# Performance work log

Measured on AMD Instinct MI355X. Metric: run time of the kernel, lower is better.

The kernel has to match this reference:

```python
import jax, jax.numpy as jnp
import numpy as np
from jax import lax

DN = ('NCHW', 'OIHW', 'NCHW')

def conv(x, w, b, stride=1, pad=0):
    y = lax.conv_general_dilated(x, w, (stride, stride), ((pad, pad), (pad, pad)), dimension_numbers=DN)
    return y + b[None, :, None, None]

def conv_transpose(x, w, b):
    # torch ConvTranspose2d(k=4, s=2, p=1): w is (in_ch, out_ch, 4, 4)
    wf = jnp.flip(w, (2, 3)).transpose(1, 0, 2, 3)  # -> (out_ch, in_ch, 4, 4)
    pad = 4 - 1 - 1  # k - 1 - p = 2
    y = lax.conv_general_dilated(x, wf, (1, 1), ((pad, pad), (pad, pad)), lhs_dilation=(2, 2), dimension_numbers=DN)
    return y + b[None, :, None, None]

def setup_inputs() -> dict:
    key = jax.random.key(0)
    ks = jax.random.split(key, 16)
    HID, ZC, K = 256, 64, 512
    def w(k, shape):
        return (jax.random.normal(k, shape, jnp.float32) * 0.02)
    z = lambda n: jnp.zeros((n,), jnp.float32)
    return {
        'x': jax.random.uniform(ks[0], (8, 3, 128, 128), jnp.float32),
        'c1_w': w(ks[1], (HID, 3, 4, 4)), 'c1_b': z(HID),
        'c2_w': w(ks[2], (HID, HID, 4, 4)), 'c2_b': z(HID),
        'r0_w3': w(ks[3], (HID, HID, 3, 3)), 'r0_b3': z(HID),
        'r0_w1': w(ks[4], (HID, HID, 1, 1)), 'r0_b1': z(HID),
        'r1_w3': w(ks[5], (HID, HID, 3, 3)), 'r1_b3': z(HID),
        'r1_w1': w(ks[6], (HID, HID, 1, 1)), 'r1_b1': z(HID),
        'to_z_w': w(ks[7], (ZC, HID, 1, 1)), 'to_z_b': z(ZC),
        'codebook': jax.random.uniform(ks[8], (K, ZC), jnp.float32, -1.0 / K, 1.0 / K),
        'from_z_w': w(ks[9], (HID, ZC, 1, 1)), 'from_z_b': z(HID),
        't1_w': w(ks[10], (HID, HID, 4, 4)), 't1_b': z(HID),
        't2_w': w(ks[11], (HID, 3, 4, 4)), 't2_b': z(3),
    }

def _vqvae(x, c1_w, c1_b, c2_w, c2_b, r0_w3, r0_b3, r0_w1, r0_b1,
           r1_w3, r1_b3, r1_w1, r1_b1, to_z_w, to_z_b, codebook,
           from_z_w, from_z_b, t1_w, t1_b, t2_w, t2_b):
    # ---- Encoder ----
    h = jax.nn.relu(conv(x, c1_w, c1_b, stride=2, pad=1))
    h = jax.nn.relu(conv(h, c2_w, c2_b, stride=2, pad=1))
    for (w3, b3, w1, b1) in ((r0_w3, r0_b3, r0_w1, r0_b1), (r1_w3, r1_b3, r1_w1, r1_b1)):
        r = conv(jax.nn.relu(h), w3, b3, pad=1)
        r = conv(jax.nn.relu(r), w1, b1)
        h = h + r
    z_e = conv(h, to_z_w, to_z_b)  # [B, ZC, H/4, W/4]
    # ---- Vector quantization ----
    B, C, H, W = z_e.shape
    z_flat = z_e.transpose(0, 2, 3, 1).reshape(-1, C)  # [N, C]
    dist = (jnp.sum(z_flat * z_flat, axis=1, keepdims=True)
            - 2.0 * z_flat @ codebook.T
            + jnp.sum(codebook * codebook, axis=1)[None, :])  # [N, K]
    ids = jnp.argmin(dist, axis=1)  # [N]
    e_k_flat = codebook[ids]  # [N, C]
    e_k_st_flat = z_flat + lax.stop_gradient(e_k_flat - z_flat)
    e_k = e_k_flat.reshape(B, H, W, C).transpose(0, 3, 1, 2)
    e_k_st = e_k_st_flat.reshape(B, H, W, C).transpose(0, 3, 1, 2)
    ids = ids.reshape(B, H, W)
    # ---- Decoder ----
    d = jax.nn.relu(conv(e_k_st, from_z_w, from_z_b))
    d = jax.nn.relu(conv_transpose(d, t1_w, t1_b))
    out = jax.nn.sigmoid(conv_transpose(d, t2_w, t2_b))
    return out, z_e, e_k, ids

def reference(x, c1_w, c1_b, c2_w, c2_b, r0_w3, r0_b3, r0_w1, r0_b1,
              r1_w3, r1_b3, r1_w1, r1_b1, to_z_w, to_z_b, codebook,
              from_z_w, from_z_b, t1_w, t1_b, t2_w, t2_b):
    return _vqvae(x, c1_w, c1_b, c2_w, c2_b, r0_w3, r0_b3, r0_w1, r0_b1,
                  r1_w3, r1_b3, r1_w1, r1_b1, to_z_w, to_z_b, codebook,
                  from_z_w, from_z_b, t1_w, t1_b, t2_w, t2_b)
```

## Files before the change

kernel.cpp:

```cpp
#include <hip/hip_runtime.h>
#include <math.h>


typedef unsigned int uint;
typedef unsigned short ushort_t;
using short8 = __attribute__((ext_vector_type(8))) short;
using f32x4  = __attribute__((ext_vector_type(4))) float;

__device__ __attribute__((aligned(16))) ushort_t g_zpad[512];

static __device__ __forceinline__ int rfl(int x) { return __builtin_amdgcn_readfirstlane(x); }
static __device__ __forceinline__ ushort_t f2bf(float f) {
  uint u = __float_as_uint(f);
  return (ushort_t)((u + 0x7fffu + ((u >> 16) & 1u)) >> 16);
}
static __device__ __forceinline__ float bf2f(ushort_t b) {
  return __uint_as_float(((uint)b) << 16);
}
static __device__ __forceinline__ void gload16(const ushort_t* g, void* l) {
  __builtin_amdgcn_global_load_lds(
      (const __attribute__((address_space(1))) void*)g,
      (__attribute__((address_space(3))) void*)l, 16, 0, 0);
}

__global__ void k_transpose_w(const float* __restrict__ w, float* __restrict__ wT, int CO, int CIKK) {
  int idx = blockIdx.x * 256 + threadIdx.x;
  if (idx >= CO * CIKK) return;
  int co = idx % CO, i = idx / CO;
  wT[idx] = w[co * CIKK + i];
}

template<int KIND>
__global__ __launch_bounds__(256) void k_prep_enc(
    const float* __restrict__ w, ushort_t* __restrict__ wp)
{
  constexpr int KK = (KIND == 0) ? 16 : (KIND == 1 ? 9 : 1);
  constexpr int KW = (KIND == 0) ? 4  : (KIND == 1 ? 3 : 1);
  constexpr int NT = KK;
  const int tid = threadIdx.x;
  const int wvg = blockIdx.x * 4 + (tid >> 6);
  const int lane = tid & 63;
  const int co = wvg >> 2;
  const int ci = (wvg & 3) * 64 + lane;
  const float* src = w + (size_t)(co * 256 + ci) * KK;
  const int coT = co >> 6, row = co & 63, cg = ci >> 5, k = ci & 31;
  float v[KK];
#pragma unroll
  for (int j = 0; j < KK; ++j) v[j] = src[j];
#pragma unroll
  for (int tap = 0; tap < NT; ++tap) {
    int ky, kx;
    if (KIND == 0)      { ky = tap >> 2; kx = tap & 3; }
    else if (KIND == 1) { ky = tap / 3;  kx = tap - ky * 3; }
    else                { ky = 0; kx = 0; }
    float val = v[ky * KW + kx];
    ushort_t b0 = f2bf(val);
    ushort_t b1 = f2bf(val - bf2f(b0));
    const int chunk = tap * 8 + cg;
    size_t base = ((size_t)(chunk * 4 + coT) << 12) + row * 32 + k;
    wp[base] = b0;
    wp[base + 2048] = b1;
  }
}

__global__ void k_prep_t1w(const float* __restrict__ w, ushort_t* __restrict__ wb) {
  int idx = blockIdx.x * 256 + threadIdx.x;
  int kk  = idx & 31;
  int co  = (idx >> 5) & 255;
  int c8  = (idx >> 13) & 7;
  int tap = (idx >> 16) & 3;
  int par = idx >> 18;
  int ry = par & 1, rx = (par >> 1) & 1;
  int a = tap >> 1, b = tap & 1;
  int ky = ((ry + 1) & 1) + 2 * a;
  int kx = ((rx + 1) & 1) + 2 * b;
  int ci = c8 * 32 + kk;
  wb[idx] = f2bf(w[((ci * 256 + co) << 4) + ky * 4 + kx]);
}

__global__ void k_prep_t2w(const float* __restrict__ w, ushort_t* __restrict__ wb) {
  int idx = blockIdx.x * 256 + threadIdx.x;
  int k = idx & 31, co = (idx >> 5) & 15, chunk = (idx >> 9) & 31, par = idx >> 14;
  int tap = chunk >> 3, cg = chunk & 7;
  int a = tap >> 1, b = tap & 1;
  int ry = par & 1, rx = (par >> 1) & 1;
  int ky = ((ry + 1) & 1) + 2 * a;
  int kx = ((rx + 1) & 1) + 2 * b;
  int ci = cg * 32 + k;
  float v = (co < 3) ? w[((ci * 3 + co) << 4) + ky * 4 + kx] : 0.f;
  wb[idx] = f2bf(v);
}

__global__ void k_prep_cb(const float* __restrict__ cb, float* __restrict__ cnorm) {
  int idx = blockIdx.x * 256 + threadIdx.x;
  if (idx < 512) {
    float s = 0.f;
    for (int c = 0; c < 64; ++c) { float v = cb[idx * 64 + c]; s = fmaf(v, v, s); }
    cnorm[idx] = s;
  }
}

__global__ __launch_bounds__(256) void k_conv1_split(
    const float* __restrict__ in, ushort_t* __restrict__ o0, ushort_t* __restrict__ o1,
    const float* __restrict__ wT, const float* __restrict__ bias)
{
  __shared__ float s_in[3 * 360];
  const int tid = threadIdx.x;
  const int lane = tid & 63;
  const int wv = rfl(tid >> 6);
  const int px = lane & 7, py = lane >> 3;
  const int tx = blockIdx.x & 7, ty = blockIdx.x >> 3;
  const int X = tx * 8, Y = ty * 8;
  const int cob = blockIdx.y * 64 + wv * 16;
  const int n = blockIdx.z;
  float acc[16];
#pragma unroll
  for (int i = 0; i < 16; ++i) acc[i] = bias[cob + i];
  const float* inN = in + (size_t)n * 3 * 16384;
  for (int e = tid; e < 3 * 360; e += 256) {
    int col2 = e % 20; int t = e / 20; int row = t % 18; int ci = t / 18;
    int pr = col2 / 10, hc = col2 % 10, ixl = 2 * hc + pr;
    int iy = 2 * Y - 1 + row, ix = 2 * X - 1 + ixl;
    float v = 0.f;
    if (ixl < 18 && (unsigned)iy < 128u && (unsigned)ix < 128u)
      v = inN[ci * 16384 + iy * 128 + ix];
    s_in[e] = v;
  }
  __syncthreads();
  const float* wc = wT + cob;
#pragma unroll
  for (int c = 0; c < 3; ++c) {
    const float* base = s_in + c * 360 + py * 40 + px;
#pragma unroll
    for (int ky = 0; ky < 4; ++ky) {
#pragma unroll
      for (int kx = 0; kx < 4; ++kx) {
        float iv = base[ky * 20 + (kx & 1) * 10 + (kx >> 1)];
        const float* w = wc + (size_t)(c * 16 + ky * 4 + kx) * 256;
#pragma unroll
        for (int i = 0; i < 16; ++i) acc[i] = fmaf(iv, w[i], acc[i]);
      }
    }
  }
  const int pxg = n * 4096 + (Y + py) * 64 + (X + px);
  uint p0[8], p1[8];
#pragma unroll
  for (int i = 0; i < 8; ++i) {
    float va = fmaxf(acc[2 * i], 0.f), vb = fmaxf(acc[2 * i + 1], 0.f);
    ushort_t a0 = f2bf(va), b0 = f2bf(vb);
    ushort_t a1 = f2bf(va - bf2f(a0)), b1 = f2bf(vb - bf2f(b0));
    p0[i] = (uint)a0 | ((uint)b0 << 16);
    p1[i] = (uint)a1 | ((uint)b1 << 16);
  }
  ushort_t* d0 = o0 + (size_t)pxg * 256 + cob;
  ushort_t* d1 = o1 + (size_t)pxg * 256 + cob;
  uint4 v0a; v0a.x = p0[0]; v0a.y = p0[1]; v0a.z = p0[2]; v0a.w = p0[3];
  uint4 v0b; v0b.x = p0[4]; v0b.y = p0[5]; v0b.z = p0[6]; v0b.w = p0[7];
  uint4 v1a; v1a.x = p1[0]; v1a.y = p1[1]; v1a.z = p1[2]; v1a.w = p1[3];
  uint4 v1b; v1b.x = p1[4]; v1b.y = p1[5]; v1b.z = p1[6]; v1b.w = p1[7];
  *(uint4*)d0 = v0a; *(uint4*)(d0 + 8) = v0b;
  *(uint4*)d1 = v1a; *(uint4*)(d1 + 8) = v1b;
}

template<int KIND>
__global__ __launch_bounds__(256) void k_enc_mfma_split(
    const ushort_t* __restrict__ x0, const ushort_t* __restrict__ x1,
    const ushort_t* __restrict__ wp, float* __restrict__ part)
{
  __shared__ ushort_t smem[2][12288];
  const int tid = threadIdx.x, lane = tid & 63, wv = tid >> 6;
  const int l15 = lane & 15, q = lane >> 4;
  const int pxT = blockIdx.x, coT = blockIdx.y;
  constexpr int NCH = (KIND == 0) ? 128 : 72;
  const int CH0 = blockIdx.z * (NCH / 2), CH1 = CH0 + NCH / 2;
  f32x4 acc[4][2];
#pragma unroll
  for (int m = 0; m < 4; ++m)
#pragma unroll
    for (int n = 0; n < 2; ++n) acc[m][n] = (f32x4){0.f, 0.f, 0.f, 0.f};

  const int r0 = tid >> 2, kq = tid & 3;
  int bimg[2], bu[2], bvc[2];
#pragma unroll
  for (int r = 0; r < 2; ++r) {
    int bpx = pxT * 128 + r0 + r * 64;
    bimg[r] = bpx >> 10; int bp = bpx & 1023; bu[r] = bp >> 5; bvc[r] = bp & 31;
  }
  const ushort_t* srcB[2][2];
  int ptap = -1;
  auto retap = [&](int tap) {
    ptap = tap;
    int ky, kx;
    if (KIND == 0) { ky = tap >> 2; kx = tap & 3; }
    else           { ky = tap / 3;  kx = tap - ky * 3; }
#pragma unroll
    for (int r = 0; r < 2; ++r) {
      bool v; size_t rowb;
      if (KIND == 0) {
        int iy = 2 * bu[r] - 1 + ky, ix = 2 * bvc[r] - 1 + kx;
        v = ((unsigned)iy < 64u) && ((unsigned)ix < 64u);
        rowb = ((size_t)(bimg[r] * 4096 + iy * 64 + ix)) << 8;
      } else {
        int iy = bu[r] - 1 + ky, ix = bvc[r] - 1 + kx;
        v = ((unsigned)iy < 32u) && ((unsigned)ix < 32u);
        rowb = ((size_t)(bimg[r] * 1024 + iy * 32 + ix)) << 8;
      }
      srcB[r][0] = (v ? (x0 + rowb) : g_zpad) + kq * 8;
      srcB[r][1] = (v ? (x1 + rowb) : g_zpad) + kq * 8;
    }
  };

  const int wvb = wv * 1024;
  auto stage = [&](int chunk, int bi) {
    const int tap = chunk >> 3, cg = chunk & 7;
    if (tap != ptap) retap(tap);
    char* bufb = (char*)smem[bi];
    const ushort_t* ap = wp + ((size_t)(chunk * 4 + coT) << 12) + tid * 8;
    gload16(ap,        bufb + wvb);
    gload16(ap + 2048, bufb + 4096 + wvb);
    const int ko = cg * 32;
    gload16(srcB[0][0] + ko, bufb + 8192 + wvb);
    gload16(srcB[1][0] + ko, bufb + 8192 + 4096 + wvb);
    gload16(srcB[0][1] + ko, bufb + 16384 + wvb);
    gload16(srcB[1][1] + ko, bufb + 16384 + 4096 + wvb);
  };
  auto compute = [&](const ushort_t* buf) {
    const ushort_t* sA = buf;
    const ushort_t* sB = buf + 4096;
    short8 af[4][2], bf[2][2];
#pragma unroll
    for (int m = 0; m < 4; ++m)
#pragma unroll
      for (int pl = 0; pl < 2; ++pl)
        af[m][pl] = *(const short8*)(sA + pl * 2048 + (m * 16 + l15) * 32 + q * 8);
#pragma unroll
    for (int n = 0; n < 2; ++n)
#pragma unroll
      for (int pl = 0; pl < 2; ++pl)
        bf[n][pl] = *(const short8*)(sB + pl * 4096 + (wv * 32 + n * 16 + l15) * 32 + q * 8);
#pragma unroll
    for (int m = 0; m < 4; ++m)
#pragma unroll
      for (int n = 0; n < 2; ++n) {
        acc[m][n] = __builtin_amdgcn_mfma_f32_16x16x32_bf16(af[m][0], bf[n][0], acc[m][n], 0, 0, 0);
        acc[m][n] = __builtin_amdgcn_mfma_f32_16x16x32_bf16(af[m][0], bf[n][1], acc[m][n], 0, 0, 0);
        acc[m][n] = __builtin_amdgcn_mfma_f32_16x16x32_bf16(af[m][1], bf[n][0], acc[m][n], 0, 0, 0);
      }
  };

  stage(CH0, 0);
  __syncthreads();
  int cur = 0;
  for (int c = CH0; c < CH1; ++c) {
    if (c + 1 < CH1) stage(c + 1, cur ^ 1);
    compute(smem[cur]);
    __syncthreads();
    cur ^= 1;
  }

  float* pz = part + ((size_t)blockIdx.z << 21);
#pragma unroll
  for (int m = 0; m < 4; ++m) {
#pragma unroll
    for (int n = 0; n < 2; ++n) {
#pragma unroll
      for (int r = 0; r < 4; ++r) {
        const int co_l = m * 16 + q * 4 + r;
        const int px_l = wv * 32 + n * 16 + l15;
        const int px = pxT * 128 + px_l;
        const int img = px >> 10, pp = px & 1023;
        const size_t ha = ((size_t)(img * 256 + coT * 64 + co_l)) * 1024 + pp;
        pz[ha] = acc[m][n][r];
      }
    }
  }
}

template<bool WH>
__global__ __launch_bounds__(256) void k_enc_epi(
    const float* __restrict__ part, float* __restrict__ h32,
    ushort_t* __restrict__ s0, ushort_t* __restrict__ s1,
    const float* __restrict__ bias)
{
  const int px = blockIdx.x * 256 + threadIdx.x;
  const int co0 = blockIdx.y * 16;
  const int img = px >> 10, pp = px & 1023;
  const float* part1 = part + (1u << 21);
  uint p0[8], p1[8];
#pragma unroll
  for (int i = 0; i < 8; ++i) {
    size_t ha = ((size_t)(img * 256 + co0 + 2 * i)) * 1024 + pp;
    size_t hb = ha + 1024;
    float va = part[ha] + part1[ha] + bias[co0 + 2 * i];
    float vb = part[hb] + part1[hb] + bias[co0 + 2 * i + 1];
    float sa, sb;
    if (WH) {
      va = fmaxf(va, 0.f); vb = fmaxf(vb, 0.f);
      h32[ha] = va; h32[hb] = vb; sa = va; sb = vb;
    } else { sa = fmaxf(va, 0.f); sb = fmaxf(vb, 0.f); }
    ushort_t a0 = f2bf(sa), b0 = f2bf(sb);
    p0[i] = (uint)a0 | ((uint)b0 << 16);
    p1[i] = (uint)f2bf(sa - bf2f(a0)) | ((uint)f2bf(sb - bf2f(b0)) << 16);
  }
  ushort_t* d0 = s0 + (size_t)px * 256 + co0;
  ushort_t* d1 = s1 + (size_t)px * 256 + co0;
  uint4 v0a; v0a.x = p0[0]; v0a.y = p0[1]; v0a.z = p0[2]; v0a.w = p0[3];
  uint4 v0b; v0b.x = p0[4]; v0b.y = p0[5]; v0b.z = p0[6]; v0b.w = p0[7];
  uint4 v1a; v1a.x = p1[0]; v1a.y = p1[1]; v1a.z = p1[2]; v1a.w = p1[3];
  uint4 v1b; v1b.x = p1[4]; v1b.y = p1[5]; v1b.z = p1[6]; v1b.w = p1[7];
  *(uint4*)d0 = v0a; *(uint4*)(d0 + 8) = v0b;
  *(uint4*)d1 = v1a; *(uint4*)(d1 + 8) = v1b;
}

template<bool WS>
__global__ __launch_bounds__(256) void k_enc_mfma(
    const ushort_t* __restrict__ x0, const ushort_t* __restrict__ x1,
    const ushort_t* __restrict__ wp, const float* __restrict__ bias,
    float* __restrict__ h32, ushort_t* __restrict__ sp0, ushort_t* __restrict__ sp1)
{
  __shared__ ushort_t smem[24576];
  const int tid = threadIdx.x, lane = tid & 63, wv = tid >> 6;
  const int l15 = lane & 15, q = lane >> 4;
  const int pxT = blockIdx.x, coT = blockIdx.y;
  f32x4 acc[4][2];
#pragma unroll
  for (int m = 0; m < 4; ++m)
#pragma unroll
    for (int n = 0; n < 2; ++n) acc[m][n] = (f32x4){0.f, 0.f, 0.f, 0.f};

  const int r0 = tid >> 2, kq = tid & 3;
  const ushort_t* srcB[2][2];
#pragma unroll
  for (int r = 0; r < 2; ++r) {
    size_t rowb = ((size_t)(pxT * 128 + r0 + r * 64)) << 8;
    srcB[r][0] = x0 + rowb + kq * 8;
    srcB[r][1] = x1 + rowb + kq * 8;
  }
  const int wvb = wv * 1024;
  auto stage = [&](int c, int bi) {
    char* bufb = (char*)(smem + bi * 12288);
    const ushort_t* ap = wp + ((size_t)(c * 4 + coT) << 12) + tid * 8;
    gload16(ap,        bufb + wvb);
    gload16(ap + 2048, bufb + 4096 + wvb);
    const int ko = c * 32;
    gload16(srcB[0][0] + ko, bufb + 8192 + wvb);
    gload16(srcB[1][0] + ko, bufb + 8192 + 4096 + wvb);
    gload16(srcB[0][1] + ko, bufb + 16384 + wvb);
    gload16(srcB[1][1] + ko, bufb + 16384 + 4096 + wvb);
  };
  auto compute = [&](const ushort_t* buf) {
    const ushort_t* sA = buf;
    const ushort_t* sB = buf + 4096;
    short8 af[4][2], bf[2][2];
#pragma unroll
    for (int m = 0; m < 4; ++m)
#pragma unroll
      for (int pl = 0; pl < 2; ++pl)
        af[m][pl] = *(const short8*)(sA + pl * 2048 + (m * 16 + l15) * 32 + q * 8);
#pragma unroll
    for (int n = 0; n < 2; ++n)
#pragma unroll
      for (int pl = 0; pl < 2; ++pl)
        bf[n][pl] = *(const short8*)(sB + pl * 4096 + (wv * 32 + n * 16 + l15) * 32 + q * 8);
#pragma unroll
    for (int m = 0; m < 4; ++m)
#pragma unroll
      for (int n = 0; n < 2; ++n) {
        acc[m][n] = __builtin_amdgcn_mfma_f32_16x16x32_bf16(af[m][0], bf[n][0], acc[m][n], 0, 0, 0);
        acc[m][n] = __builtin_amdgcn_mfma_f32_16x16x32_bf16(af[m][0], bf[n][1], acc[m][n], 0, 0, 0);
        acc[m][n] = __builtin_amdgcn_mfma_f32_16x16x32_bf16(af[m][1], bf[n][0], acc[m][n], 0, 0, 0);
      }
  };

  stage(0, 0);
  __syncthreads();
  int cur = 0;
  for (int c = 0; c < 8; ++c) {
    if (c + 1 < 8) stage(c + 1, cur ^ 1);
    compute(smem + cur * 12288);
    __syncthreads();
    cur ^= 1;
  }

#pragma unroll
  for (int m = 0; m < 4; ++m) {
#pragma unroll
    for (int n = 0; n < 2; ++n) {
#pragma unroll
      for (int r = 0; r < 4; ++r) {
        const int co_l = m * 16 + q * 4 + r;
        const int px_l = wv * 32 + n * 16 + l15;
        float v = acc[m][n][r] + bias[coT * 64 + co_l];
        const int px = pxT * 128 + px_l;
        const int img = px >> 10, pp = px & 1023;
        const size_t ha = ((size_t)(img * 256 + coT * 64 + co_l)) * 1024 + pp;
        v += h32[ha];
        h32[ha] = v;
        if (WS) {
          float sv = fmaxf(v, 0.f);
          ushort_t b0 = f2bf(sv);
          smem[px_l * 72 + co_l] = b0;
          smem[9216 + px_l * 72 + co_l] = f2bf(sv - bf2f(b0));
        }
      }
    }
  }
  if (WS) {
    __syncthreads();
#pragma unroll
    for (int i = 0; i < 8; ++i) {
      int idx = tid + 256 * i;
      int pl = idx >> 10, w2 = idx & 1023, pxl = w2 >> 3, g = w2 & 7;
      uint4 vv = *(const uint4*)(smem + pl * 9216 + pxl * 72 + g * 8);
      ushort_t* dst = (pl ? sp1 : sp0) + ((size_t)(pxT * 128 + pxl)) * 256 + coT * 64 + g * 8;
      *(uint4*)dst = vv;
    }
  }
}

__global__ __launch_bounds__(256) void k_conv1x1(
    const float* __restrict__ in, float* __restrict__ out,
    const float* __restrict__ wT, const float* __restrict__ bias,
    int CI, int CO, int P)
{
  const int p = blockIdx.x * 256 + threadIdx.x;
  const int cob = blockIdx.y * 16;
  const int n = blockIdx.z;
  const float* inN = in + (size_t)n * CI * P + p;
  float acc[16];
#pragma unroll
  for (int i = 0; i < 16; ++i) acc[i] = bias[cob + i];
  const float* wr = wT + cob;
#pragma unroll 4
  for (int ci = 0; ci < CI; ++ci) {
    float iv = inN[(size_t)ci * P];
    const float* w = wr + (size_t)ci * CO;
#pragma unroll
    for (int i = 0; i < 16; ++i) acc[i] = fmaf(iv, w[i], acc[i]);
  }
  float* outN = out + (size_t)n * CO * P + p;
#pragma unroll
  for (int i = 0; i < 16; ++i) outN[(size_t)(cob + i) * P] = acc[i];
}

__global__ __launch_bounds__(256) void k_vq_part(
    const float* __restrict__ z_e, const float* __restrict__ cb,
    const float* __restrict__ cnorm, float* __restrict__ pbest, int* __restrict__ pbid)
{
  int g = blockIdx.x * 256 + threadIdx.x;
  int chunk = blockIdx.y;
  int img = g >> 10, p = g & 1023;
  const float* zp = z_e + (size_t)img * 64 * 1024 + p;
  float z[64];
#pragma unroll
  for (int c = 0; c < 64; ++c) z[c] = zp[(size_t)c * 1024];
  float best = 3.4e38f; int bid = chunk << 5;
  const int j0 = chunk << 5;
  for (int j = j0; j < j0 + 32; ++j) {
    const float* cj = cb + j * 64;
    float m = 0.f;
#pragma unroll
    for (int c = 0; c < 64; ++c) m = fmaf(z[c], cj[c], m);
    float d = fmaf(-2.f, m, cnorm[j]);
    if (d < best) { best = d; bid = j; }
  }
  pbest[chunk * 8192 + g] = best;
  pbid[chunk * 8192 + g] = bid;
}

__global__ __launch_bounds__(256) void k_vq_reduce(
    const float* __restrict__ pbest, const int* __restrict__ pbid,
    const float* __restrict__ cb, float* __restrict__ ids_f, float* __restrict__ ek)
{
  int g = blockIdx.x * 256 + threadIdx.x;
  float best = 3.4e38f; int bid = 0;
#pragma unroll
  for (int ch = 0; ch < 16; ++ch) {
    float d = pbest[ch * 8192 + g];
    int b = pbid[ch * 8192 + g];
    if (d < best) { best = d; bid = b; }
  }
  ids_f[g] = (float)bid;
  int img = g >> 10, p = g & 1023;
  const float* cbid = cb + bid * 64;
  float* ekp = ek + (size_t)img * 64 * 1024 + p;
#pragma unroll
  for (int c = 0; c < 64; ++c) ekp[(size_t)c * 1024] = cbid[c];
}

__global__ __launch_bounds__(256) void k_from_z(
    const float* __restrict__ ek, ushort_t* __restrict__ nhwc,
    const float* __restrict__ wT, const float* __restrict__ bias)
{
  const int p = blockIdx.x * 256 + threadIdx.x;
  const int co0 = blockIdx.y * 16;
  const int n = blockIdx.z;
  const float* inN = ek + (size_t)n * 64 * 1024 + p;
  float acc[16];
#pragma unroll
  for (int i = 0; i < 16; ++i) acc[i] = bias[co0 + i];
#pragma unroll 4
  for (int ci = 0; ci < 64; ++ci) {
    float iv = inN[(size_t)ci * 1024];
    const float* w = wT + (size_t)ci * 256 + co0;
#pragma unroll
    for (int i = 0; i < 16; ++i) acc[i] = fmaf(iv, w[i], acc[i]);
  }
  uint pk[8];
#pragma unroll
  for (int i = 0; i < 8; ++i) {
    ushort_t lo = f2bf(fmaxf(acc[2 * i], 0.f));
    ushort_t hi = f2bf(fmaxf(acc[2 * i + 1], 0.f));
    pk[i] = (uint)lo | ((uint)hi << 16);
  }
  ushort_t* op = nhwc + (((size_t)n * 1024 + p) * 256 + co0);
  uint4 v0; v0.x = pk[0]; v0.y = pk[1]; v0.z = pk[2]; v0.w = pk[3];
  uint4 v1; v1.x = pk[4]; v1.y = pk[5]; v1.z = pk[6]; v1.w = pk[7];
  *(uint4*)(op) = v0;
  *(uint4*)(op + 8) = v1;
}

__global__ __launch_bounds__(256) void k_mfma_t1(
    const ushort_t* __restrict__ nhwc, const ushort_t* __restrict__ wb,
    const float* __restrict__ bias, ushort_t* __restrict__ t1o)
{
  __shared__ ushort_t smem[2][8192];
  const int tid = threadIdx.x;
  const int lane = tid & 63;
  const int wv = tid >> 6;
  const int wm = wv & 1, wn = wv >> 1;
  const int l15 = lane & 15, q = lane >> 4;
  const int pxT = blockIdx.x, coT = blockIdx.y, par = blockIdx.z;
  const int ry = par & 1, rx = (par >> 1) & 1;
  const int pxbase = pxT * 128;
  const int img = pxbase >> 10;
  f32x4 acc[4][4];
#pragma unroll
  for (int i = 0; i < 4; ++i)
#pragma unroll
    for (int j = 0; j < 4; ++j) acc[i][j] = (f32x4){0.f, 0.f, 0.f, 0.f};

  const int srow = tid >> 2, kg = tid & 3;
  int bu2[2], bv2[2];
#pragma unroll
  for (int r = 0; r < 2; ++r) {
    int px = pxbase + srow + r * 64;
    bu2[r] = (px >> 5) & 31; bv2[r] = px & 31;
  }
  const ushort_t* nb[2];
  int ptap = -1;
  auto retap = [&](int tap) {
    ptap = tap;
    int ta = tap >> 1, tb = tap & 1;
#pragma unroll
    for (int r = 0; r < 2; ++r) {
      int iy = bu2[r] + ry - ta, ix = bv2[r] + rx - tb;
      bool v = ((unsigned)iy < 32u) && ((unsigned)ix < 32u);
      nb[r] = (v ? (nhwc + (((size_t)(img * 1024 + iy * 32 + ix)) << 8)) : g_zpad) + kg * 8;
    }
  };
  const int wvb = wv * 1024;
  auto stage = [&](int c, int bi) {
    const int tap = c >> 3, c8 = c & 7;
    if (tap != ptap) retap(tap);
    char* bufb = (char*)smem[bi];
    const ushort_t* Abase = wb + ((size_t)((par * 4 + tap) * 8 + c8) << 13) + coT * 4096 + tid * 8;
    gload16(Abase,        bufb + wvb);
    gload16(Abase + 2048, bufb + 4096 + wvb);
    const int ko = c8 * 32;
    gload16(nb[0] + ko, bufb + 8192 + wvb);
    gload16(nb[1] + ko, bufb + 8192 + 4096 + wvb);
  };
  auto compute = [&](const ushort_t* buf) {
    const ushort_t* sA = buf;
    const ushort_t* sB = buf + 4096;
    short8 af[4], bfr[4];
#pragma unroll
    for (int i = 0; i < 4; ++i)
      af[i] = *(const short8*)(sA + (wm * 64 + i * 16 + l15) * 32 + q * 8);
#pragma unroll
    for (int j = 0; j < 4; ++j)
      bfr[j] = *(const short8*)(sB + (wn * 64 + j * 16 + l15) * 32 + q * 8);
#pragma unroll
    for (int i = 0; i < 4; ++i)
#pragma unroll
      for (int j = 0; j < 4; ++j)
        acc[i][j] = __builtin_amdgcn_mfma_f32_16x16x32_bf16(af[i], bfr[j], acc[i][j], 0, 0, 0);
  };

  stage(0, 0);
  __syncthreads();
  int cur = 0;
  for (int c = 0; c < 32; ++c) {
    if (c + 1 < 32) stage(c + 1, cur ^ 1);
    compute(smem[cur]);
    __syncthreads();
    cur ^= 1;
  }

#pragma unroll
  for (int i = 0; i < 4; ++i) {
    int co = coT * 128 + wm * 64 + i * 16 + q * 4;
#pragma unroll
    for (int j = 0; j < 4; ++j) {
      int px = pxbase + wn * 64 + j * 16 + l15;
      int u = (px >> 5) & 31, vv = px & 31;
      int oy = 2 * u + ry, ox = 2 * vv + rx;
      ushort_t e0 = f2bf(fmaxf(acc[i][j][0] + bias[co + 0], 0.f));
      ushort_t e1 = f2bf(fmaxf(acc[i][j][1] + bias[co + 1], 0.f));
      ushort_t e2 = f2bf(fmaxf(acc[i][j][2] + bias[co + 2], 0.f));
      ushort_t e3 = f2bf(fmaxf(acc[i][j][3] + bias[co + 3], 0.f));
      uint2 pk; pk.x = (uint)e0 | ((uint)e1 << 16); pk.y = (uint)e2 | ((uint)e3 << 16);
      *(uint2*)(t1o + ((size_t)(img * 4096 + oy * 64 + ox) * 256 + co)) = pk;
    }
  }
}

__global__ __launch_bounds__(256) void k_mfma_t2(
    const ushort_t* __restrict__ t1o, const ushort_t* __restrict__ wb,
    const float* __restrict__ bias, float* __restrict__ out)
{
  __shared__ ushort_t sA2[256 * 32];
  __shared__ ushort_t sB2[16 * 32];
  const int tid = threadIdx.x, lane = tid & 63, wv = tid >> 6;
  const int l15 = lane & 15, q = lane >> 4;
  const int pxb = blockIdx.x * 256;
  const int par = blockIdx.y;
  const int ry = par & 1, rx = (par >> 1) & 1;
  f32x4 acc[4];
#pragma unroll
  for (int m = 0; m < 4; ++m) acc[m] = (f32x4){0.f, 0.f, 0.f, 0.f};
  const int kg = tid & 3;
  const int ssw = ((tid >> 2) & 7) << 3;
  size_t rb[4]; bool rv[4];
  for (int chunk = 0; chunk < 32; ++chunk) {
    const int tap = chunk >> 3, cg = chunk & 7;
    const int a = tap >> 1, b = tap & 1;
    if ((chunk & 7) == 0) {
#pragma unroll
      for (int i = 0; i < 4; ++i) {
        int row = (tid >> 2) + 64 * i;
        int px = pxb + row;
        int img = px >> 12, p = px & 4095, u = p >> 6, v = p & 63;
        int iy = u + ry - a, ix = v + rx - b;
        rv[i] = ((unsigned)iy < 64u) && ((unsigned)ix < 64u);
        rb[i] = ((size_t)(img * 4096 + iy * 64 + ix)) << 8;
      }
    }
    uint4 av[4];
#pragma unroll
    for (int i = 0; i < 4; ++i) {
      if (rv[i]) av[i] = *(const uint4*)(t1o + rb[i] + cg * 32 + kg * 8);
      else { av[i].x = 0; av[i].y = 0; av[i].z = 0; av[i].w = 0; }
    }
    uint4 bv;
    if (tid < 64) bv = *(const uint4*)(wb + ((size_t)(par * 32 + chunk)) * 512 + tid * 8);
    __syncthreads();
#pragma unroll
    for (int i = 0; i < 4; ++i)
      *(uint4*)(sA2 + (((((tid >> 2) + 64 * i) * 32) + kg * 8) ^ ssw)) = av[i];
    if (tid < 64) *(uint4*)(sB2 + ((tid * 8) ^ ssw)) = bv;
    __syncthreads();
    short8 bf = *(const short8*)(sB2 + ((l15 * 32 + q * 8) ^ ((l15 & 7) << 3)));
#pragma unroll
    for (int m = 0; m < 4; ++m) {
      const int row = wv * 64 + m * 16 + l15;
      short8 af = *(const short8*)(sA2 + ((row * 32 + q * 8) ^ ((row & 7) << 3)));
      acc[m] = __builtin_amdgcn_mfma_f32_16x16x32_bf16(af, bf, acc[m], 0, 0, 0);
    }
    __syncthreads();
  }
  const int co = l15;
  if (co < 3) {
    float bco = bias[co];
#pragma unroll
    for (int m = 0; m < 4; ++m) {
#pragma unroll
      for (int r = 0; r < 4; ++r) {
        int px = pxb + wv * 64 + m * 16 + q * 4 + r;
        int img = px >> 12, p = px & 4095, u = p >> 6, v = p & 63;
        size_t addr = ((size_t)(img * 3 + co)) * 16384 + (2 * u + ry) * 128 + (2 * v + rx);
        out[addr] = 1.f / (1.f + expf(-(acc[m][r] + bco)));
      }
    }
  }
}

extern "C" void kernel_launch(void* const* d_in, const int* in_sizes, int n_in,
                              void* d_out, int out_size, void* d_ws, size_t ws_size,
                              hipStream_t stream) {
  (void)in_sizes; (void)n_in; (void)out_size; (void)ws_size;
  const float* x      = (const float*)d_in[0];
  const float* c1_w   = (const float*)d_in[1];
  const float* c1_b   = (const float*)d_in[2];
  const float* c2_w   = (const float*)d_in[3];
  const float* c2_b   = (const float*)d_in[4];
  const float* r0_w3  = (const float*)d_in[5];
  const float* r0_b3  = (const float*)d_in[6];
  const float* r0_w1  = (const float*)d_in[7];
  const float* r0_b1  = (const float*)d_in[8];
  const float* r1_w3  = (const float*)d_in[9];
  const float* r1_b3  = (const float*)d_in[10];
  const float* r1_w1  = (const float*)d_in[11];
  const float* r1_b1  = (const float*)d_in[12];
  const float* to_z_w = (const float*)d_in[13];
  const float* to_z_b = (const float*)d_in[14];
  const float* cb     = (const float*)d_in[15];
  const float* from_z_w = (const float*)d_in[16];
  const float* from_z_b = (const float*)d_in[17];
  const float* t1_w   = (const float*)d_in[18];
  const float* t1_b   = (const float*)d_in[19];
  const float* t2_w   = (const float*)d_in[20];
  const float* t2_b   = (const float*)d_in[21];

  float* wsf = (float*)d_ws;
  ushort_t* xs1p0 = (ushort_t*)(wsf + 0);
  ushort_t* xs1p1 = (ushort_t*)(wsf + 4194304);
  float*    cp0   = wsf + 8388608;
  float*    h32   = wsf + 8388608;
  float*    qp0   = wsf + 4194304;
  ushort_t* sE0   = (ushort_t*)(wsf + 0);
  ushort_t* sE1   = (ushort_t*)(wsf + 1048576);
  ushort_t* sF0   = (ushort_t*)(wsf + 2097152);
  ushort_t* sF1   = (ushort_t*)(wsf + 3145728);
  float*    pbest = wsf + 0;
  int*      pbid  = (int*)(wsf + 131072);
  ushort_t* t1out = (ushort_t*)(wsf + 2097152);
  ushort_t* decn  = (ushort_t*)(wsf + 6291456);
  ushort_t* wp_c2   = (ushort_t*)(wsf + 12582912);
  ushort_t* wp_r0w3 = (ushort_t*)(wsf + 13631488);
  ushort_t* wp_r1w3 = (ushort_t*)(wsf + 14221312);
  ushort_t* wp_r0w1 = (ushort_t*)(wsf + 14811136);
  ushort_t* wp_r1w1 = (ushort_t*)(wsf + 14876672);
  float*    wt_c1   = wsf + 14942208;
  float*    wt_toz  = wsf + 14954496;
  float*    wt_fromz= wsf + 14970880;
  ushort_t* t1wb    = (ushort_t*)(wsf + 14987264);
  ushort_t* w2pk    = (ushort_t*)(wsf + 15511552);
  float*    cnorm   = wsf + 15544320;

  float* out_img = (float*)d_out;
  float* z_e_out = out_img + 393216;
  float* e_k_out = z_e_out + 524288;
  float* ids_out = e_k_out + 524288;

  k_transpose_w<<<48, 256, 0, stream>>>(c1_w, wt_c1, 256, 48);
  k_transpose_w<<<64, 256, 0, stream>>>(to_z_w, wt_toz, 64, 256);
  k_transpose_w<<<64, 256, 0, stream>>>(from_z_w, wt_fromz, 256, 64);
  k_prep_enc<0><<<256, 256, 0, stream>>>(c2_w,  wp_c2);
  k_prep_enc<1><<<256, 256, 0, stream>>>(r0_w3, wp_r0w3);
  k_prep_enc<1><<<256, 256, 0, stream>>>(r1_w3, wp_r1w3);
  k_prep_enc<2><<<256, 256, 0, stream>>>(r0_w1, wp_r0w1);
  k_prep_enc<2><<<256, 256, 0, stream>>>(r1_w1, wp_r1w1);
  k_prep_t1w<<<4096, 256, 0, stream>>>(t1_w, t1wb);
  k_prep_t2w<<<256, 256, 0, stream>>>(t2_w, w2pk);
  k_prep_cb<<<2, 256, 0, stream>>>(cb, cnorm);

  k_conv1_split<<<dim3(64, 4, 8), 256, 0, stream>>>(x, xs1p0, xs1p1, wt_c1, c1_b);
  k_enc_mfma_split<0><<<dim3(64, 4, 2), 256, 0, stream>>>(xs1p0, xs1p1, wp_c2, cp0);
  k_enc_epi<true><<<dim3(32, 16), 256, 0, stream>>>(cp0, h32, sE0, sE1, c2_b);
  k_enc_mfma_split<1><<<dim3(64, 4, 2), 256, 0, stream>>>(sE0, sE1, wp_r0w3, qp0);
  k_enc_epi<false><<<dim3(32, 16), 256, 0, stream>>>(qp0, nullptr, sE0, sE1, r0_b3);
  k_enc_mfma<true ><<<dim3(64, 4), 256, 0, stream>>>(
      sE0, sE1, wp_r0w1, r0_b1, h32, sF0, sF1);
  k_enc_mfma_split<1><<<dim3(64, 4, 2), 256, 0, stream>>>(sF0, sF1, wp_r1w3, qp0);
  k_enc_epi<false><<<dim3(32, 16), 256, 0, stream>>>(qp0, nullptr, sE0, sE1, r1_b3);
  k_enc_mfma<false><<<dim3(64, 4), 256, 0, stream>>>(
      sE0, sE1, wp_r1w1, r1_b1, h32, nullptr, nullptr);
  k_conv1x1<<<dim3(4, 4, 8), 256, 0, stream>>>(h32, z_e_out, wt_toz, to_z_b, 256, 64, 1024);

  k_vq_part<<<dim3(32, 16), 256, 0, stream>>>(z_e_out, cb, cnorm, pbest, pbid);
  k_vq_reduce<<<32, 256, 0, stream>>>(pbest, pbid, cb, ids_out, e_k_out);

  k_from_z<<<dim3(4, 16, 8), 256, 0, stream>>>(e_k_out, decn, wt_fromz, from_z_b);
  k_mfma_t1<<<dim3(64, 2, 4), 256, 0, stream>>>(decn, t1wb, t1_b, t1out);
  k_mfma_t2<<<dim3(128, 4), 256, 0, stream>>>(t1out, w2pk, t2_b, out_img);
}
```

Before: 426.3 us.

## Add halo-tiled 3x3 MFMA conv kernel and merge weight prep launches

```diff
diff --git a/kernel.cpp b/kernel.cpp
--- a/kernel.cpp
+++ b/kernel.cpp
@@ -23,11 +23,45 @@
       (__attribute__((address_space(3))) void*)l, 16, 0, 0);
 }
 
-__global__ void k_transpose_w(const float* __restrict__ w, float* __restrict__ wT, int CO, int CIKK) {
-  int idx = blockIdx.x * 256 + threadIdx.x;
-  if (idx >= CO * CIKK) return;
-  int co = idx % CO, i = idx / CO;
-  wT[idx] = w[co * CIKK + i];
+__global__ __launch_bounds__(256) void k_prep_misc(
+    const float* __restrict__ c1w, float* __restrict__ wt_c1,
+    const float* __restrict__ tozw, float* __restrict__ wt_toz,
+    const float* __restrict__ fromzw, float* __restrict__ wt_fromz,
+    const float* __restrict__ cb, float* __restrict__ cnorm,
+    const float* __restrict__ t2w, ushort_t* __restrict__ w2pk)
+{
+  const int b = blockIdx.x, tid = threadIdx.x;
+  if (b < 48) {
+    int idx = b * 256 + tid;
+    int co = idx % 256, i = idx / 256;
+    wt_c1[idx] = c1w[co * 48 + i];
+  } else if (b < 112) {
+    int idx = (b - 48) * 256 + tid;
+    int co = idx % 64, i = idx / 64;
+    wt_toz[idx] = tozw[co * 256 + i];
+  } else if (b < 176) {
+    int idx = (b - 112) * 256 + tid;
+    int co = idx % 256, i = idx / 256;
+    wt_fromz[idx] = fromzw[co * 64 + i];
+  } else if (b < 178) {
+    int idx = (b - 176) * 256 + tid;
+    if (idx < 512) {
+      float s = 0.f;
+      for (int c = 0; c < 64; ++c) { float v = cb[idx * 64 + c]; s = fmaf(v, v, s); }
+      cnorm[idx] = s;
+    }
+  } else {
+    int idx = (b - 178) * 256 + tid;
+    int k = idx & 31, co = (idx >> 5) & 15, chunk = (idx >> 9) & 31, par = idx >> 14;
+    int tap = chunk >> 3, cg = chunk & 7;
+    int a = tap >> 1, bb = tap & 1;
+    int ry = par & 1, rx = (par >> 1) & 1;
+    int ky = ((ry + 1) & 1) + 2 * a;
+    int kx = ((rx + 1) & 1) + 2 * bb;
+    int ci = cg * 32 + k;
+    float v = (co < 3) ? t2w[((ci * 3 + co) << 4) + ky * 4 + kx] : 0.f;
+    w2pk[idx] = f2bf(v);
+  }
 }
 
 template<int KIND>
@@ -39,6 +73,43 @@
   constexpr int NT = KK;
   const int tid = threadIdx.x;
   const int wvg = blockIdx.x * 4 + (tid >> 6);
+  const int lane = tid & 63;
+  const int co = wvg >> 2;
+  const int ci = (wvg & 3) * 64 + lane;
+  const float* src = w + (size_t)(co * 256 + ci) * KK;
+  const int coT = co >> 6, row = co & 63, cg = ci >> 5, k = ci & 31;
+  float v[KK];
+#pragma unroll
+  for (int j = 0; j < KK; ++j) v[j] = src[j];
+#pragma unroll
+  for (int tap = 0; tap < NT; ++tap) {
+    int ky, kx;
+    if (KIND == 0)      { ky = tap >> 2; kx = tap & 3; }
+    else if (KIND == 1) { ky = tap / 3;  kx = tap - ky * 3; }
+    else                { ky = 0; kx = 0; }
+    float val = v[ky * KW + kx];
+    ushort_t b0 = f2bf(val);
+    ushort_t b1 = f2bf(val - bf2f(b0));
+    const int chunk = tap * 8 + cg;
+    size_t base = ((size_t)(chunk * 4 + coT) << 12) + row * 32 + k;
+    wp[base] = b0;
+    wp[base + 2048] = b1;
+  }
+}
+
+template<int KIND>
+__global__ __launch_bounds__(256) void k_prep_enc2(
+    const float* __restrict__ wa, ushort_t* __restrict__ oa,
+    const float* __restrict__ wb2, ushort_t* __restrict__ ob)
+{
+  constexpr int KK = (KIND == 0) ? 16 : (KIND == 1 ? 9 : 1);
+  constexpr int KW = (KIND == 0) ? 4  : (KIND == 1 ? 3 : 1);
+  constexpr int NT = KK;
+  const float* w = (blockIdx.x < 256) ? wa : wb2;
+  ushort_t* wp = (blockIdx.x < 256) ? oa : ob;
+  const int bx = blockIdx.x & 255;
+  const int tid = threadIdx.x;
+  const int wvg = bx * 4 + (tid >> 6);
   const int lane = tid & 63;
   const int co = wvg >> 2;
   const int ci = (wvg & 3) * 64 + lane;
@@ -76,28 +147,6 @@
   int kx = ((rx + 1) & 1) + 2 * b;
   int ci = c8 * 32 + kk;
   wb[idx] = f2bf(w[((ci * 256 + co) << 4) + ky * 4 + kx]);
-}
-
-__global__ void k_prep_t2w(const float* __restrict__ w, ushort_t* __restrict__ wb) {
-  int idx = blockIdx.x * 256 + threadIdx.x;
-  int k = idx & 31, co = (idx >> 5) & 15, chunk = (idx >> 9) & 31, par = idx >> 14;
-  int tap = chunk >> 3, cg = chunk & 7;
-  int a = tap >> 1, b = tap & 1;
-  int ry = par & 1, rx = (par >> 1) & 1;
-  int ky = ((ry + 1) & 1) + 2 * a;
-  int kx = ((rx + 1) & 1) + 2 * b;
-  int ci = cg * 32 + k;
-  float v = (co < 3) ? w[((ci * 3 + co) << 4) + ky * 4 + kx] : 0.f;
-  wb[idx] = f2bf(v);
-}
-
-__global__ void k_prep_cb(const float* __restrict__ cb, float* __restrict__ cnorm) {
-  int idx = blockIdx.x * 256 + threadIdx.x;
-  if (idx < 512) {
-    float s = 0.f;
-    for (int c = 0; c < 64; ++c) { float v = cb[idx * 64 + c]; s = fmaf(v, v, s); }
-    cnorm[idx] = s;
-  }
 }
 
 __global__ __launch_bounds__(256) void k_conv1_split(
@@ -270,6 +319,103 @@
         const int px = pxT * 128 + px_l;
         const int img = px >> 10, pp = px & 1023;
         const size_t ha = ((size_t)(img * 256 + coT * 64 + co_l)) * 1024 + pp;
+        pz[ha] = acc[m][n][r];
+      }
+    }
+  }
+}
+
+__global__ __launch_bounds__(256) void k_enc_mfma_3x3h(
+    const ushort_t* __restrict__ x0, const ushort_t* __restrict__ x1,
+    const ushort_t* __restrict__ wp, float* __restrict__ part)
+{
+  __shared__ ushort_t smem[32768];
+  const int tid = threadIdx.x, lane = tid & 63, wv = tid >> 6;
+  const int l15 = lane & 15, q = lane >> 4;
+  const int pxT = blockIdx.x, coT = blockIdx.y;
+  const int CG0 = blockIdx.z * 4;
+  const int img = pxT >> 3;
+  const int U0 = (pxT & 7) * 4;
+  f32x4 acc[2][2];
+#pragma unroll
+  for (int m = 0; m < 2; ++m)
+#pragma unroll
+    for (int n = 0; n < 2; ++n) acc[m][n] = (f32x4){0.f, 0.f, 0.f, 0.f};
+
+  const ushort_t* srcp[7];
+#pragma unroll
+  for (int i = 0; i < 7; ++i) {
+    int slot = i * 256 + tid;
+    int pl = slot >= 816 ? 1 : 0;
+    int rem = slot - pl * 816;
+    int rr = rem / 136;
+    int c4 = rem - rr * 136;
+    int cc = c4 >> 2, kq2 = c4 & 3;
+    int iy = U0 - 1 + rr, ix = cc - 1;
+    bool valid = (slot < 1632) && ((unsigned)iy < 32u) && ((unsigned)ix < 32u);
+    const ushort_t* base = valid
+        ? ((pl ? x1 : x0) + (((size_t)(img * 1024 + iy * 32 + ix)) << 8))
+        : g_zpad;
+    srcp[i] = base + kq2 * 8;
+  }
+  const int apl = tid >> 7;
+  const int aus = apl * 2048 + (coT & 1) * 1024 + (tid & 127) * 8;
+  const int coTq = coT >> 1;
+  const int wvb = wv * 1024;
+  char* bufb = (char*)smem;
+
+  for (int cg = CG0; cg < CG0 + 4; ++cg) {
+#pragma unroll
+    for (int tap = 0; tap < 9; ++tap) {
+      const int chunk = tap * 8 + cg;
+      gload16(wp + ((size_t)(chunk * 4 + coTq) << 12) + aus, bufb + tap * 4096 + wvb);
+    }
+    const int ko = cg * 32;
+#pragma unroll
+    for (int i = 0; i < 7; ++i)
+      gload16(srcp[i] + ko, bufb + 36864 + i * 4096 + wvb);
+    __syncthreads();
+    const ushort_t* Ab = smem;
+    const ushort_t* Hb = smem + 18432;
+#pragma unroll 3
+    for (int tap = 0; tap < 9; ++tap) {
+      const int ky = tap / 3, kx = tap - ky * 3;
+      short8 af[2][2], bf[2][2];
+#pragma unroll
+      for (int m = 0; m < 2; ++m)
+#pragma unroll
+        for (int pl = 0; pl < 2; ++pl)
+          af[m][pl] = *(const short8*)(Ab + tap * 2048 + pl * 1024 + (m * 16 + l15) * 32 + q * 8);
+      const int r = wv + ky;
+#pragma unroll
+      for (int n = 0; n < 2; ++n)
+#pragma unroll
+        for (int pl = 0; pl < 2; ++pl)
+          bf[n][pl] = *(const short8*)(Hb + pl * 6528 + r * 1088 + (n * 16 + l15 + kx) * 32 + q * 8);
+#pragma unroll
+      for (int m = 0; m < 2; ++m)
+#pragma unroll
+        for (int n = 0; n < 2; ++n) {
+          acc[m][n] = __builtin_amdgcn_mfma_f32_16x16x32_bf16(af[m][0], bf[n][0], acc[m][n], 0, 0, 0);
+          acc[m][n] = __builtin_amdgcn_mfma_f32_16x16x32_bf16(af[m][0], bf[n][1], acc[m][n], 0, 0, 0);
+          acc[m][n] = __builtin_amdgcn_mfma_f32_16x16x32_bf16(af[m][1], bf[n][0], acc[m][n], 0, 0, 0);
+        }
+    }
+    __syncthreads();
+  }
+
+  float* pz = part + ((size_t)blockIdx.z << 21);
+#pragma unroll
+  for (int m = 0; m < 2; ++m) {
+#pragma unroll
+    for (int n = 0; n < 2; ++n) {
+#pragma unroll
+      for (int r = 0; r < 4; ++r) {
+        const int co_l = m * 16 + q * 4 + r;
+        const int px_l = wv * 32 + n * 16 + l15;
+        const int px = pxT * 128 + px_l;
+        const int imgp = px >> 10, pp = px & 1023;
+        const size_t ha = ((size_t)(imgp * 256 + coT * 32 + co_l)) * 1024 + pp;
         pz[ha] = acc[m][n][r];
       }
     }
@@ -744,26 +890,21 @@
   float* e_k_out = z_e_out + 524288;
   float* ids_out = e_k_out + 524288;
 
-  k_transpose_w<<<48, 256, 0, stream>>>(c1_w, wt_c1, 256, 48);
-  k_transpose_w<<<64, 256, 0, stream>>>(to_z_w, wt_toz, 64, 256);
-  k_transpose_w<<<64, 256, 0, stream>>>(from_z_w, wt_fromz, 256, 64);
-  k_prep_enc<0><<<256, 256, 0, stream>>>(c2_w,  wp_c2);
-  k_prep_enc<1><<<256, 256, 0, stream>>>(r0_w3, wp_r0w3);
-  k_prep_enc<1><<<256, 256, 0, stream>>>(r1_w3, wp_r1w3);
-  k_prep_enc<2><<<256, 256, 0, stream>>>(r0_w1, wp_r0w1);
-  k_prep_enc<2><<<256, 256, 0, stream>>>(r1_w1, wp_r1w1);
+  k_prep_misc<<<434, 256, 0, stream>>>(c1_w, wt_c1, to_z_w, wt_toz,
+                                       from_z_w, wt_fromz, cb, cnorm, t2_w, w2pk);
+  k_prep_enc<0><<<256, 256, 0, stream>>>(c2_w, wp_c2);
+  k_prep_enc2<1><<<512, 256, 0, stream>>>(r0_w3, wp_r0w3, r1_w3, wp_r1w3);
+  k_prep_enc2<2><<<512, 256, 0, stream>>>(r0_w1, wp_r0w1, r1_w1, wp_r1w1);
   k_prep_t1w<<<4096, 256, 0, stream>>>(t1_w, t1wb);
-  k_prep_t2w<<<256, 256, 0, stream>>>(t2_w, w2pk);
-  k_prep_cb<<<2, 256, 0, stream>>>(cb, cnorm);
 
   k_conv1_split<<<dim3(64, 4, 8), 256, 0, stream>>>(x, xs1p0, xs1p1, wt_c1, c1_b);
   k_enc_mfma_split<0><<<dim3(64, 4, 2), 256, 0, stream>>>(xs1p0, xs1p1, wp_c2, cp0);
   k_enc_epi<true><<<dim3(32, 16), 256, 0, stream>>>(cp0, h32, sE0, sE1, c2_b);
-  k_enc_mfma_split<1><<<dim3(64, 4, 2), 256, 0, stream>>>(sE0, sE1, wp_r0w3, qp0);
+  k_enc_mfma_3x3h<<<dim3(64, 8, 2), 256, 0, stream>>>(sE0, sE1, wp_r0w3, qp0);
   k_enc_epi<false><<<dim3(32, 16), 256, 0, stream>>>(qp0, nullptr, sE0, sE1, r0_b3);
   k_enc_mfma<true ><<<dim3(64, 4), 256, 0, stream>>>(
       sE0, sE1, wp_r0w1, r0_b1, h32, sF0, sF1);
-  k_enc_mfma_split<1><<<dim3(64, 4, 2), 256, 0, stream>>>(sF0, sF1, wp_r1w3, qp0);
+  k_enc_mfma_3x3h<<<dim3(64, 8, 2), 256, 0, stream>>>(sF0, sF1, wp_r1w3, qp0);
   k_enc_epi<false><<<dim3(32, 16), 256, 0, stream>>>(qp0, nullptr, sE0, sE1, r1_b3);
   k_enc_mfma<false><<<dim3(64, 4), 256, 0, stream>>>(
       sE0, sE1, wp_r1w1, r1_b1, h32, nullptr, nullptr);
```

After: 409.4 us. -4.0%, faster.
